# Optimization experiments

Measured on AMD Instinct MI355X. Metric: run time of the kernel, lower is better.

The kernel has to match this reference:

```python
import jax, jax.numpy as jnp
import numpy as np
import math

T = 120      # frame_num == audio_len == max_seq_len
D = 64       # hidden_layer_size
H = 2        # n_head
DH = D // H
DFF = 2 * D
DOUT = 31
PERIOD = 10
EPS = 1e-5
NEG = -1e9
SCALE = 1.0 / math.sqrt(DH)
SLOPES = (1.0 / 16.0, 1.0 / 256.0)  # ALiBi slopes for n_head=2


def _pe():
    # PeriodicPositionalEncoding: sinusoid over one period, tiled
    pos = jnp.arange(PERIOD, dtype=jnp.float32)[:, None]
    div = jnp.exp(jnp.arange(0, D, 2, dtype=jnp.float32) * (-math.log(10000.0) / D))
    s, c = jnp.sin(pos * div), jnp.cos(pos * div)
    pe = jnp.stack([s, c], axis=-1).reshape(PERIOD, D)  # interleave sin/cos
    return jnp.tile(pe, (T // PERIOD + 1, 1))[:T]


def _alibi_mask():
    # causal mask + ALiBi bias: alibi[i,j] = -slope * floor((i-j)/period) for j<=i
    slopes = jnp.array(SLOPES, dtype=jnp.float32)
    i = jnp.arange(T)[:, None]
    j = jnp.arange(T)[None, :]
    rel = ((i - j) // PERIOD).astype(jnp.float32)
    return jnp.where(j <= i, -slopes[:, None, None] * rel, NEG)  # [H,T,T]


def _ln(x, g, b):
    m = x.mean(-1, keepdims=True)
    v = ((x - m) ** 2).mean(-1, keepdims=True)
    return (x - m) / jnp.sqrt(v + EPS) * g + b


def setup_inputs() -> dict:
    key = jax.random.key(0)
    ks = iter(jax.random.split(key, 32))
    n = lambda shape, s=0.05: jax.random.normal(next(ks), shape, dtype=jnp.float32) * s
    inp = {
        'audio': jax.random.normal(next(ks), (1, T, 1024), dtype=jnp.float32),
        'W_audio': n((D, 1024)), 'b_audio': n((D,)),
        'obj_W': n((D, 5)),
        'Wq': n((D, D)), 'bq': n((D,)), 'Wk': n((D, D)), 'bk': n((D,)),
        'Wv': n((D, D)), 'bv': n((D,)), 'Wo': n((D, D)), 'bo': n((D,)),
        'Wv2': n((D, D)), 'bv2': n((D,)), 'Wo2': n((D, D)), 'bo2': n((D,)),
        'g1': jnp.ones((D,)), 'be1': jnp.zeros((D,)),
        'g2': jnp.ones((D,)), 'be2': jnp.zeros((D,)),
        'g3': jnp.ones((D,)), 'be3': jnp.zeros((D,)),
        'W1': n((DFF, D)), 'c1': n((DFF,)), 'W2': n((D, DFF)), 'c2': n((D,)),
        'Wr': n((DOUT, D)), 'br': n((DOUT,)), 'Wm': n((D, DOUT)), 'bm': n((D,)),
    }
    return inp


def _forward(audio, W_audio, b_audio, obj_W, Wq, bq, Wk, bk, Wv, bv, Wo, bo,
             Wv2, bv2, Wo2, bo2, g1, be1, g2, be2, g3, be3,
             W1, c1, W2, c2, Wr, br, Wm, bm):
    mem = audio[0] @ W_audio.T + b_audio          # [S,D], S == T
    style = obj_W[:, 0]                            # obj_vector @ [1,0,0,0,0]
    pe = _pe()
    mask = _alibi_mask()
    slopes = jnp.array(SLOPES, dtype=jnp.float32)
    jarr = jnp.arange(T)

    # enc_dec_mask leaves exactly one memory key per target row (anti-diagonal
    # from the end); the feedback row t at step t always attends memory[-1],
    # so its cross-attn output is just the projected value of the last frame.
    cross_last = (mem[-1] @ Wv2.T + bv2) @ Wo2.T + bo2  # [D]

    def step(emb, t):
        # decode only the last row (row t) of the growing sequence; 1-layer
        # post-norm decoder => row t depends only on input rows 0..t.
        x = emb + pe                                 # PPE over prefix
        xq = jnp.take(x, t, axis=0)                  # [D]
        q = (xq @ Wq.T + bq).reshape(H, DH)
        k = (x @ Wk.T + bk).reshape(T, H, DH)
        v = (x @ Wv.T + bv).reshape(T, H, DH)
        bias = jnp.where(jarr <= t,
                         -slopes[:, None] * ((t - jarr) // PERIOD).astype(jnp.float32),
                         NEG)                        # [H,T]
        sc = jnp.einsum('hd,shd->hs', q, k) * SCALE + bias
        a = jax.nn.softmax(sc, axis=-1)
        sa = jnp.einsum('hs,shd->hd', a, v).reshape(D) @ Wo.T + bo
        h1 = _ln(xq + sa, g1, be1)
        h2 = _ln(h1 + cross_last, g2, be2)
        h3 = _ln(h2 + jax.nn.relu(h2 @ W1.T + c1) @ W2.T + c2, g3, be3)
        new = (h3 @ Wr.T + br) @ Wm.T + bm + style   # vertice_map(vertice_map_r(.)) + style
        emb = jax.lax.dynamic_update_slice(emb, new[None, :], (t + 1, 0))
        return emb, None

    emb0 = jnp.zeros((T, D), audio.dtype).at[0].set(style)
    emb, _ = jax.lax.scan(step, emb0, jnp.arange(T - 1))

    # final full-length decode (last loop iteration of the torch module)
    x = emb + pe
    q = (x @ Wq.T + bq).reshape(T, H, DH)
    k = (x @ Wk.T + bk).reshape(T, H, DH)
    v = (x @ Wv.T + bv).reshape(T, H, DH)
    sc = jnp.einsum('thd,shd->hts', q, k) * SCALE + mask
    a = jax.nn.softmax(sc, axis=-1)
    sa = jnp.einsum('hts,shd->thd', a, v).reshape(T, D) @ Wo.T + bo
    h1 = _ln(x + sa, g1, be1)
    # at length T with S == T the enc_dec_mask aligns target row j <-> memory row j
    cross = (mem @ Wv2.T + bv2) @ Wo2.T + bo2
    h2 = _ln(h1 + cross, g2, be2)
    h3 = _ln(h2 + jax.nn.relu(h2 @ W1.T + c1) @ W2.T + c2, g3, be3)
    return (h3 @ Wr.T + br)[None]                    # [1,T,31]


def reference(audio, W_audio, b_audio, obj_W, Wq, bq, Wk, bk, Wv, bv, Wo, bo,
              Wv2, bv2, Wo2, bo2, g1, be1, g2, be2, g3, be3,
              W1, c1, W2, c2, Wr, br, Wm, bm):
    return _forward(audio, W_audio, b_audio, obj_W, Wq, bq, Wk, bk, Wv, bv, Wo, bo,
                    Wv2, bv2, Wo2, bo2, g1, be1, g2, be2, g3, be3,
                    W1, c1, W2, c2, Wr, br, Wm, bm)
```

## Files before the change

### kernel.cpp

```cpp
#include <hip/hip_runtime.h>

typedef unsigned short u16;
typedef unsigned int   u32;
typedef _Float16 f16;
typedef f16 h2 __attribute__((ext_vector_type(2)));
typedef f16 h4 __attribute__((ext_vector_type(4)));
typedef f16 h8 __attribute__((ext_vector_type(8)));

#define T_    120
#define D_    64
#define DFF_  128
#define DOUT_ 31
#define KROW_ 68
#define VROW_ 132

#if defined(__has_builtin)
#if __has_builtin(__builtin_amdgcn_fdot2)
#define DOT2(a,b,c) __builtin_amdgcn_fdot2((a),(b),(c),false)
#endif
#endif
#ifndef DOT2
#define DOT2(a,b,c) ((float)(a).x*(float)(b).x + ((float)(a).y*(float)(b).y + (c)))
#endif
#define SHV(x,i,j) __builtin_shufflevector((x),(x),(i),(j))

__device__ __forceinline__ h2 pk(float a, float b){
#if defined(__has_builtin) && __has_builtin(__builtin_amdgcn_cvt_pkrtz)
  return __builtin_bit_cast(h2, __builtin_amdgcn_cvt_pkrtz(a, b));
#else
  h2 r; r.x = (f16)a; r.y = (f16)b; return r;
#endif
}

__device__ __forceinline__ float b2f(u16 u){ return __uint_as_float(((u32)u) << 16); }
__device__ __forceinline__ float2 bp2(u32 u){
  float2 r; r.x = __uint_as_float(u << 16); r.y = __uint_as_float(u & 0xffff0000u); return r;
}
__device__ __forceinline__ u16 f2bu(float f){
  u32 u = __float_as_uint(f);
  u32 r = u + 0x7fffu + ((u >> 16) & 1u);
  return (u16)(r >> 16);
}
#define WSYNC() do{ __asm__ __volatile__("" ::: "memory"); __builtin_amdgcn_wave_barrier(); }while(0)

__device__ __forceinline__ float dpp_sum(float x){
  int t;
  t = __builtin_amdgcn_update_dpp(0, __float_as_int(x), 0x111, 0xf, 0xf, true); x += __int_as_float(t);
  t = __builtin_amdgcn_update_dpp(0, __float_as_int(x), 0x112, 0xf, 0xf, true); x += __int_as_float(t);
  t = __builtin_amdgcn_update_dpp(0, __float_as_int(x), 0x114, 0xf, 0xf, true); x += __int_as_float(t);
  t = __builtin_amdgcn_update_dpp(0, __float_as_int(x), 0x118, 0xf, 0xf, true); x += __int_as_float(t);
  t = __builtin_amdgcn_update_dpp(0, __float_as_int(x), 0x142, 0xf, 0xf, true); x += __int_as_float(t);
  t = __builtin_amdgcn_update_dpp(0, __float_as_int(x), 0x143, 0xf, 0xf, true); x += __int_as_float(t);
  return __int_as_float(__builtin_amdgcn_readlane(__float_as_int(x), 63));
}
__device__ __forceinline__ float dpp_max_pos(float x){
  int t;
  t = __builtin_amdgcn_update_dpp(0, __float_as_int(x), 0x111, 0xf, 0xf, true); x = fmaxf(x, __int_as_float(t));
  t = __builtin_amdgcn_update_dpp(0, __float_as_int(x), 0x112, 0xf, 0xf, true); x = fmaxf(x, __int_as_float(t));
  t = __builtin_amdgcn_update_dpp(0, __float_as_int(x), 0x114, 0xf, 0xf, true); x = fmaxf(x, __int_as_float(t));
  t = __builtin_amdgcn_update_dpp(0, __float_as_int(x), 0x118, 0xf, 0xf, true); x = fmaxf(x, __int_as_float(t));
  t = __builtin_amdgcn_update_dpp(0, __float_as_int(x), 0x142, 0xf, 0xf, true); x = fmaxf(x, __int_as_float(t));
  t = __builtin_amdgcn_update_dpp(0, __float_as_int(x), 0x143, 0xf, 0xf, true); x = fmaxf(x, __int_as_float(t));
  return __int_as_float(__builtin_amdgcn_readlane(__float_as_int(x), 63));
}
__device__ __forceinline__ float pe_val(int row, int i){
  const float coef = -0.28782313662425574f;
  int p = row % 10;
  float dv  = __expf((float)(i >> 1) * coef);
  float ang = (float)p * dv;
  return (i & 1) ? __cosf(ang) : __sinf(ang);
}
__device__ __forceinline__ void loadrow32(h2* dst, const float* row){
  #pragma unroll
  for (int r = 0; r < 16; ++r){
    float4 f = ((const float4*)row)[r];
    dst[2*r]   = pk(f.x, f.y);
    dst[2*r+1] = pk(f.z, f.w);
  }
}
__device__ __forceinline__ void loadrow64(h2* dst, const float* row){
  #pragma unroll
  for (int r = 0; r < 32; ++r){
    float4 f = ((const float4*)row)[r];
    dst[2*r]   = pk(f.x, f.y);
    dst[2*r+1] = pk(f.z, f.w);
  }
}

__global__ __launch_bounds__(256) void k_prep(const float* __restrict__ Wv, const float* __restrict__ Wo,
                                              const float* __restrict__ W1, const float* __restrict__ W2,
                                              const float* __restrict__ Wr,
                                              u16* __restrict__ wvb, u16* __restrict__ wob,
                                              u16* __restrict__ w1b, u16* __restrict__ w2b,
                                              u16* __restrict__ wrb){
  int i0 = blockIdx.x*256 + threadIdx.x, stride = gridDim.x*256;
  for (int i = i0; i < 4096; i += stride){ wvb[i] = f2bu(Wv[i]); wob[i] = f2bu(Wo[i]); }
  for (int i = i0; i < 8192; i += stride){ w1b[i] = f2bu(W1[i]); w2b[i] = f2bu(W2[i]); }
  for (int i = i0; i < 1984; i += stride){ wrb[i] = f2bu(Wr[i]); }
}

__global__ __launch_bounds__(256) void k_mem(const float* __restrict__ audio,
                                             const float* __restrict__ Wa,
                                             const float* __restrict__ ba,
                                             float* __restrict__ mem){
  __shared__ float ash[1024];
  const int t = blockIdx.x, tid = threadIdx.x;
  for (int i = tid; i < 1024; i += 256) ash[i] = audio[t*1024 + i];
  __syncthreads();
  const int w = tid >> 6, lane = tid & 63;
  for (int d = w*16; d < w*16 + 16; ++d){
    const float4* row = (const float4*)(Wa + d*1024);
    float acc = 0.f;
    #pragma unroll
    for (int m = 0; m < 4; ++m){
      float4 wp = row[lane + 64*m];
      int j = 4*(lane + 64*m);
      acc += wp.x*ash[j] + wp.y*ash[j+1] + wp.z*ash[j+2] + wp.w*ash[j+3];
    }
    acc = dpp_sum(acc);
    if (lane == 0) mem[t*64 + d] = acc + ba[d];
  }
}

__global__ __launch_bounds__(64) void k_cross(const float* __restrict__ mem,
                                              const float* __restrict__ Wv2, const float* __restrict__ bv2,
                                              const float* __restrict__ Wo2, const float* __restrict__ bo2,
                                              float* __restrict__ cross){
  __shared__ float msh[64], tsh[64];
  const int t = blockIdx.x, i = threadIdx.x;
  msh[i] = mem[t*64 + i];
  __syncthreads();
  const float4* r1 = (const float4*)(Wv2 + i*64);
  float a = bv2[i];
  #pragma unroll
  for (int j = 0; j < 16; ++j){ float4 w = r1[j]; a += w.x*msh[4*j] + w.y*msh[4*j+1] + w.z*msh[4*j+2] + w.w*msh[4*j+3]; }
  tsh[i] = a;
  __syncthreads();
  const float4* r2 = (const float4*)(Wo2 + i*64);
  float c = bo2[i];
  #pragma unroll
  for (int j = 0; j < 16; ++j){ float4 w = r2[j]; c += w.x*tsh[4*j] + w.y*tsh[4*j+1] + w.z*tsh[4*j+2] + w.w*tsh[4*j+3]; }
  cross[t*64 + i] = c;
}

__global__ __launch_bounds__(128, 1) void k_scan(
    const float* __restrict__ objW,
    const float* __restrict__ Wq, const float* __restrict__ bq,
    const float* __restrict__ Wk, const float* __restrict__ bk,
    const float* __restrict__ Wv, const float* __restrict__ bv,
    const float* __restrict__ Wo, const float* __restrict__ bo,
    const float* __restrict__ g1, const float* __restrict__ be1,
    const float* __restrict__ g2, const float* __restrict__ be2,
    const float* __restrict__ g3, const float* __restrict__ be3,
    const float* __restrict__ W1, const float* __restrict__ c1,
    const float* __restrict__ W2, const float* __restrict__ c2,
    const float* __restrict__ Wr, const float* __restrict__ br,
    const float* __restrict__ Wm, const float* __restrict__ bm,
    const float* __restrict__ cross,
    float* __restrict__ xw, float* __restrict__ Kw, float* __restrict__ Vw)
{
  __shared__ __align__(16) f16 KcS[128*KROW_];
  __shared__ __align__(16) f16 VcS[D_*VROW_];
  __shared__ __align__(16) f16 sch[256];
  __shared__ __align__(16) f16 xh[64], qh[64], ath[64], h2h[64], h3h[64], rsh[32];
  __shared__ __align__(16) f16 fsh[128];
  __shared__ float at_p[64];
  __shared__ float pe_tab[640];

  const int tid = threadIdx.x;
  const int i = tid & 63;
  const bool w0 = tid < 64;

  h2 WA[32];
  h2 WB[32];
  h2 WOr[32], W1r[32], WRr[32], WMr[16];
  h2 W2r[64];
  float biasA=0.f, biasB=0.f, bo_r=0.f, c1r=0.f, c2_r=0.f, br_r=0.f, bmst=0.f, cls_r=0.f;
  float g1r=0.f,b1r=0.f,g2r=0.f,b2r=0.f,g3r=0.f,b3r=0.f, xr=0.f;

  if (w0){
    loadrow32(WA,  Wq + i*64);
    loadrow32(WB,  Wv + i*64);
    loadrow32(WOr, Wo + i*64);
    loadrow32(W1r, W1 + i*64);
    loadrow64(W2r, W2 + i*128);
    loadrow32(WRr, Wr + (i < 31 ? i : 30)*64);
    { const float* row = Wm + i*31;
      #pragma unroll
      for (int r = 0; r < 15; ++r) WMr[r] = pk(row[2*r], row[2*r+1]);
      WMr[15] = pk(row[30], 0.f); }
    biasA = bq[i]; biasB = bv[i]; bo_r = bo[i]; c1r = c1[i]; c2_r = c2[i];
    br_r = (i < 31) ? br[i] : 0.f;
    float st = objW[i*5];
    bmst = bm[i] + st;
    cls_r = cross[119*64 + i];
    g1r=g1[i]; b1r=be1[i]; g2r=g2[i]; b2r=be2[i]; g3r=g3[i]; b3r=be3[i];
    xr = st + pe_val(0, i);
    xh[i] = (f16)xr;
    xw[i] = xr;
  } else {
    loadrow32(WA, Wk + i*64);
    loadrow32(WB, W1 + (64+i)*64);
    biasA = bk[i]; c1r = c1[64+i];
  }
  { u32* kcw = (u32*)KcS; for (int idx = tid; idx < 128*KROW_/2; idx += 128) kcw[idx] = 0; }
  { u32* vcw = (u32*)VcS; for (int idx = tid; idx < D_*VROW_/2;  idx += 128) vcw[idx] = 0; }
  for (int idx = tid; idx < 640; idx += 128) pe_tab[idx] = pe_val(idx >> 6, idx & 63);
  if (tid < 32) rsh[tid] = (f16)0.f;
  __syncthreads();

  int pp = 1;
  for (int t = 0; t < T_-1; ++t){
    float atp0 = 0.f;
    {
      const h8* xv = (const h8*)xh;
      float a0=biasA, a1=0.f, a2=0.f, a3=0.f;
      #pragma unroll
      for (int r = 0; r < 8; ++r){
        h8 x = xv[r];
        a0 = DOT2(WA[4*r+0], SHV(x,0,1), a0);
        a1 = DOT2(WA[4*r+1], SHV(x,2,3), a1);
        a2 = DOT2(WA[4*r+2], SHV(x,4,5), a2);
        a3 = DOT2(WA[4*r+3], SHV(x,6,7), a3);
      }
      float accA = (a0+a1)+(a2+a3);
      if (w0){
        float b0=biasB, b1=0.f, b2=0.f, b3=0.f;
        #pragma unroll
        for (int r = 0; r < 8; ++r){
          h8 x = xv[r];
          b0 = DOT2(WB[4*r+0], SHV(x,0,1), b0);
          b1 = DOT2(WB[4*r+1], SHV(x,2,3), b1);
          b2 = DOT2(WB[4*r+2], SHV(x,4,5), b2);
          b3 = DOT2(WB[4*r+3], SHV(x,6,7), b3);
        }
        float accB = (b0+b1)+(b2+b3);
        qh[i] = (f16)accA;
        VcS[i*VROW_ + t] = (f16)accB;
        Vw[t*64 + i] = accB;
      } else {
        KcS[t*KROW_ + i] = (f16)accA;
        Kw[t*64 + i] = accA;
      }
    }
    __syncthreads();
    {
      const int h = tid >> 6, j = i;
      const h8* qv = (const h8*)(qh + h*32);
      const h4* k0 = (const h4*)(KcS + j*KROW_ + h*32);
      const h4* k1 = (const h4*)(KcS + (j+64)*KROW_ + h*32);
      float d0a=0.f,d0b=0.f,d1a=0.f,d1b=0.f;
      #pragma unroll
      for (int r = 0; r < 4; ++r){
        h8 q = qv[r];
        h4 ka = k0[2*r], kb = k0[2*r+1], kc = k1[2*r], kd = k1[2*r+1];
        d0a = DOT2(SHV(ka,0,1), SHV(q,0,1), d0a);
        d0b = DOT2(SHV(ka,2,3), SHV(q,2,3), d0b);
        d0a = DOT2(SHV(kb,0,1), SHV(q,4,5), d0a);
        d0b = DOT2(SHV(kb,2,3), SHV(q,6,7), d0b);
        d1a = DOT2(SHV(kc,0,1), SHV(q,0,1), d1a);
        d1b = DOT2(SHV(kc,2,3), SHV(q,2,3), d1b);
        d1a = DOT2(SHV(kd,0,1), SHV(q,4,5), d1a);
        d1b = DOT2(SHV(kd,2,3), SHV(q,6,7), d1b);
      }
      float d0 = d0a + d0b, d1 = d1a + d1b;
      const float slope = h ? 0.00390625f : 0.0625f;
      int r0 = (t - j) / 10, r1 = (t - j - 64) / 10;
      float s0 = (j      <= t) ? d0*0.17677669529663687f - slope*(float)r0 : -1e30f;
      float s1 = (j + 64 <= t) ? d1*0.17677669529663687f - slope*(float)r1 : -1e30f;
      float m = dpp_max_pos(fmaxf(s0, s1) + 16384.f) - 16384.f;
      float e0 = (j      <= t) ? __expf(s0 - m) : 0.f;
      float e1 = (j + 64 <= t) ? __expf(s1 - m) : 0.f;
      float inv = 1.f / dpp_sum(e0 + e1);
      sch[h*128 + j]      = (f16)(e0*inv);
      sch[h*128 + j + 64] = (f16)(e1*inv);
    }
    __syncthreads();
    {
      const int hd = i >> 5;
      const h8* av = (const h8*)(sch + hd*128) + (w0 ? 0 : 8);
      const h4* vv = (const h4*)(VcS + i*VROW_) + (w0 ? 0 : 16);
      float p0=0.f,p1=0.f,p2=0.f,p3=0.f;
      #pragma unroll
      for (int r = 0; r < 8; ++r){
        h8 a = av[r];
        h4 va = vv[2*r], vb = vv[2*r+1];
        p0 = DOT2(SHV(va,0,1), SHV(a,0,1), p0);
        p1 = DOT2(SHV(va,2,3), SHV(a,2,3), p1);
        p2 = DOT2(SHV(vb,0,1), SHV(a,4,5), p2);
        p3 = DOT2(SHV(vb,2,3), SHV(a,6,7), p3);
      }
      float p = (p0+p1)+(p2+p3);
      if (!w0) at_p[i] = p; else atp0 = p;
    }
    __syncthreads();
    if (w0){
      float atv = atp0 + at_p[i];
      ath[i] = (f16)atv;
      WSYNC();
      const h8* av = (const h8*)ath;
      float a0=bo_r, a1=0.f, a2=0.f, a3=0.f;
      #pragma unroll
      for (int r = 0; r < 8; ++r){
        h8 x = av[r];
        a0 = DOT2(WOr[4*r+0], SHV(x,0,1), a0);
        a1 = DOT2(WOr[4*r+1], SHV(x,2,3), a1);
        a2 = DOT2(WOr[4*r+2], SHV(x,4,5), a2);
        a3 = DOT2(WOr[4*r+3], SHV(x,6,7), a3);
      }
      float y = xr + (a0+a1)+(a2+a3);
      float s = dpp_sum(y), s2 = dpp_sum(y*y);
      float m = s*(1.f/64.f), var = fmaxf(s2*(1.f/64.f) - m*m, 0.f);
      float h1 = (y - m)*rsqrtf(var + 1e-5f)*g1r + b1r;
      float z = h1 + cls_r;
      float sz = dpp_sum(z), sz2 = dpp_sum(z*z);
      float mz = sz*(1.f/64.f), vz = fmaxf(sz2*(1.f/64.f) - mz*mz, 0.f);
      float h2v = (z - mz)*rsqrtf(vz + 1e-5f)*g2r + b2r;
      h2h[i] = (f16)h2v;
      at_p[i] = h2v;
    }
    __syncthreads();
    {
      const h8* hv = (const h8*)h2h;
      float a0=c1r, a1=0.f, a2=0.f, a3=0.f;
      if (w0){
        #pragma unroll
        for (int r = 0; r < 8; ++r){
          h8 x = hv[r];
          a0 = DOT2(W1r[4*r+0], SHV(x,0,1), a0);
          a1 = DOT2(W1r[4*r+1], SHV(x,2,3), a1);
          a2 = DOT2(W1r[4*r+2], SHV(x,4,5), a2);
          a3 = DOT2(W1r[4*r+3], SHV(x,6,7), a3);
        }
      } else {
        #pragma unroll
        for (int r = 0; r < 8; ++r){
          h8 x = hv[r];
          a0 = DOT2(WB[4*r+0], SHV(x,0,1), a0);
          a1 = DOT2(WB[4*r+1], SHV(x,2,3), a1);
          a2 = DOT2(WB[4*r+2], SHV(x,4,5), a2);
          a3 = DOT2(WB[4*r+3], SHV(x,6,7), a3);
        }
      }
      fsh[tid] = (f16)fmaxf((a0+a1)+(a2+a3), 0.f);
    }
    __syncthreads();
    if (w0){
      const h8* fv = (const h8*)fsh;
      float a0=c2_r, a1=0.f, a2=0.f, a3=0.f;
      #pragma unroll
      for (int r = 0; r < 16; ++r){
        h8 x = fv[r];
        a0 = DOT2(W2r[4*r+0], SHV(x,0,1), a0);
        a1 = DOT2(W2r[4*r+1], SHV(x,2,3), a1);
        a2 = DOT2(W2r[4*r+2], SHV(x,4,5), a2);
        a3 = DOT2(W2r[4*r+3], SHV(x,6,7), a3);
      }
      float y = at_p[i] + (a0+a1)+(a2+a3);
      float s = dpp_sum(y), s2 = dpp_sum(y*y);
      float m = s*(1.f/64.f), var = fmaxf(s2*(1.f/64.f) - m*m, 0.f);
      float h3v = (y - m)*rsqrtf(var + 1e-5f)*g3r + b3r;
      h3h[i] = (f16)h3v;
      WSYNC();
      const h8* h3v8 = (const h8*)h3h;
      float r0=br_r, r1=0.f, r2=0.f, r3=0.f;
      #pragma unroll
      for (int r = 0; r < 8; ++r){
        h8 x = h3v8[r];
        r0 = DOT2(WRr[4*r+0], SHV(x,0,1), r0);
        r1 = DOT2(WRr[4*r+1], SHV(x,2,3), r1);
        r2 = DOT2(WRr[4*r+2], SHV(x,4,5), r2);
        r3 = DOT2(WRr[4*r+3], SHV(x,6,7), r3);
      }
      if (i < 31) rsh[i] = (f16)((r0+r1)+(r2+r3));
      WSYNC();
      const h8* rv = (const h8*)rsh;
      float m0=bmst, m1=0.f, m2=0.f, m3=0.f;
      #pragma unroll
      for (int r = 0; r < 4; ++r){
        h8 x = rv[r];
        m0 = DOT2(WMr[4*r+0], SHV(x,0,1), m0);
        m1 = DOT2(WMr[4*r+1], SHV(x,2,3), m1);
        m2 = DOT2(WMr[4*r+2], SHV(x,4,5), m2);
        m3 = DOT2(WMr[4*r+3], SHV(x,6,7), m3);
      }
      float xn = (m0+m1)+(m2+m3) + pe_tab[pp*64 + i];
      xr = xn;
      xh[i] = (f16)xn;
      xw[(t+1)*64 + i] = xn;
    }
    __syncthreads();
    pp = (pp == 9) ? 0 : pp + 1;
  }
  {
    const h8* xv = (const h8*)xh;
    if (w0){
      float b0=biasB, b1=0.f, b2=0.f, b3=0.f;
      #pragma unroll
      for (int r = 0; r < 8; ++r){
        h8 x = xv[r];
        b0 = DOT2(WB[4*r+0], SHV(x,0,1), b0);
        b1 = DOT2(WB[4*r+1], SHV(x,2,3), b1);
        b2 = DOT2(WB[4*r+2], SHV(x,4,5), b2);
        b3 = DOT2(WB[4*r+3], SHV(x,6,7), b3);
      }
      Vw[119*64 + i] = (b0+b1)+(b2+b3);
    } else {
      float a0=biasA, a1=0.f, a2=0.f, a3=0.f;
      #pragma unroll
      for (int r = 0; r < 8; ++r){
        h8 x = xv[r];
        a0 = DOT2(WA[4*r+0], SHV(x,0,1), a0);
        a1 = DOT2(WA[4*r+1], SHV(x,2,3), a1);
        a2 = DOT2(WA[4*r+2], SHV(x,4,5), a2);
        a3 = DOT2(WA[4*r+3], SHV(x,6,7), a3);
      }
      Kw[119*64 + i] = (a0+a1)+(a2+a3);
    }
  }
}

__global__ __launch_bounds__(128) void k_final(
    const float* __restrict__ Wq, const float* __restrict__ bq, const float* __restrict__ bo,
    const float* __restrict__ g1, const float* __restrict__ be1,
    const float* __restrict__ g2, const float* __restrict__ be2,
    const float* __restrict__ g3, const float* __restrict__ be3,
    const float* __restrict__ c1, const float* __restrict__ c2, const float* __restrict__ br,
    const u16* __restrict__ wo_b, const u16* __restrict__ w1_b,
    const u16* __restrict__ w2_b, const u16* __restrict__ wr_b,
    const float* __restrict__ cross, const float* __restrict__ xw,
    const float* __restrict__ Kw, const float* __restrict__ Vw,
    float* __restrict__ out)
{
  __shared__ float xs[64], qs[64], at[64], h2s[64], h3s[64], fs[128], sc[256];
  const int irow = blockIdx.x, tid = threadIdx.x;
  if (tid < 64) xs[tid] = xw[irow*64 + tid];
  __syncthreads();
  if (tid < 64){
    const float4* wr_ = (const float4*)(Wq + tid*64);
    float acc = bq[tid];
    #pragma unroll
    for (int j = 0; j < 16; ++j){ float4 w = wr_[j]; acc += w.x*xs[4*j] + w.y*xs[4*j+1] + w.z*xs[4*j+2] + w.w*xs[4*j+3]; }
    qs[tid] = acc;
  }
  __syncthreads();
  {
    const int h = tid >> 6, j = tid & 63;
    const float* qh_ = qs + h*32;
    float d0 = 0.f, d1 = 0.f;
    const float4* k0 = (const float4*)(Kw + j*64 + h*32);
    #pragma unroll
    for (int w = 0; w < 8; ++w){ float4 p = k0[w]; d0 += p.x*qh_[4*w] + p.y*qh_[4*w+1] + p.z*qh_[4*w+2] + p.w*qh_[4*w+3]; }
    if (j < 56){
      const float4* k1 = (const float4*)(Kw + (j+64)*64 + h*32);
      #pragma unroll
      for (int w = 0; w < 8; ++w){ float4 p = k1[w]; d1 += p.x*qh_[4*w] + p.y*qh_[4*w+1] + p.z*qh_[4*w+2] + p.w*qh_[4*w+3]; }
    }
    const float slope = h ? 0.00390625f : 0.0625f;
    float s0 = (j      <= irow) ? d0*0.17677669529663687f - slope*(float)((irow-j)/10)    : -1e30f;
    float s1 = (j + 64 <= irow) ? d1*0.17677669529663687f - slope*(float)((irow-j-64)/10) : -1e30f;
    float m = dpp_max_pos(fmaxf(s0, s1) + 16384.f) - 16384.f;
    float e0 = (j      <= irow) ? __expf(s0 - m) : 0.f;
    float e1 = (j + 64 <= irow) ? __expf(s1 - m) : 0.f;
    float inv = 1.f / dpp_sum(e0 + e1);
    sc[h*128 + j]      = e0*inv;
    sc[h*128 + j + 64] = e1*inv;
  }
  __syncthreads();
  if (tid < 64){
    const float* a = sc + (tid >> 5)*128;
    float a0=0.f,a1=0.f,a2=0.f,a3=0.f;
    #pragma unroll
    for (int jj = 0; jj < 30; ++jj){
      a0 += a[4*jj]   * Vw[(4*jj)*64   + tid];
      a1 += a[4*jj+1] * Vw[(4*jj+1)*64 + tid];
      a2 += a[4*jj+2] * Vw[(4*jj+2)*64 + tid];
      a3 += a[4*jj+3] * Vw[(4*jj+3)*64 + tid];
    }
    at[tid] = (a0+a1)+(a2+a3);
  }
  __syncthreads();
  if (tid < 64){
    const u32* orow = (const u32*)(wo_b + tid*64);
    float acc = bo[tid];
    #pragma unroll
    for (int w = 0; w < 32; ++w){ float2 p = bp2(orow[w]); acc += p.x*at[2*w] + p.y*at[2*w+1]; }
    float y = xs[tid] + acc;
    float s = dpp_sum(y), s2 = dpp_sum(y*y);
    float m = s*(1.f/64.f), var = fmaxf(s2*(1.f/64.f) - m*m, 0.f);
    float h1 = (y - m)*rsqrtf(var + 1e-5f)*g1[tid] + be1[tid];
    float z = h1 + cross[irow*64 + tid];
    float sz = dpp_sum(z), sz2 = dpp_sum(z*z);
    float mz = sz*(1.f/64.f), vz = fmaxf(sz2*(1.f/64.f) - mz*mz, 0.f);
    h2s[tid] = (z - mz)*rsqrtf(vz + 1e-5f)*g2[tid] + be2[tid];
  }
  __syncthreads();
  {
    const u32* w1r = (const u32*)(w1_b + tid*64);
    float acc = c1[tid];
    #pragma unroll
    for (int w = 0; w < 32; ++w){ float2 p = bp2(w1r[w]); acc += p.x*h2s[2*w] + p.y*h2s[2*w+1]; }
    fs[tid] = fmaxf(acc, 0.f);
  }
  __syncthreads();
  if (tid < 64){
    const u32* w2r = (const u32*)(w2_b + tid*128);
    float acc = c2[tid];
    #pragma unroll
    for (int w = 0; w < 64; ++w){ float2 p = bp2(w2r[w]); acc += p.x*fs[2*w] + p.y*fs[2*w+1]; }
    float y = h2s[tid] + acc;
    float s = dpp_sum(y), s2 = dpp_sum(y*y);
    float m = s*(1.f/64.f), var = fmaxf(s2*(1.f/64.f) - m*m, 0.f);
    h3s[tid] = (y - m)*rsqrtf(var + 1e-5f)*g3[tid] + be3[tid];
  }
  __syncthreads();
  if (tid < DOUT_){
    const u32* rr = (const u32*)(wr_b + tid*64);
    float acc = br[tid];
    #pragma unroll
    for (int w = 0; w < 32; ++w){ float2 p = bp2(rr[w]); acc += p.x*h3s[2*w] + p.y*h3s[2*w+1]; }
    out[irow*DOUT_ + tid] = acc;
  }
}

extern "C" void kernel_launch(void* const* d_in, const int* in_sizes, int n_in,
                              void* d_out, int out_size, void* d_ws, size_t ws_size,
                              hipStream_t stream){
  const float* audio=(const float*)d_in[0];
  const float* Wa   =(const float*)d_in[1];
  const float* ba   =(const float*)d_in[2];
  const float* objW =(const float*)d_in[3];
  const float* Wq   =(const float*)d_in[4];
  const float* bq   =(const float*)d_in[5];
  const float* Wk   =(const float*)d_in[6];
  const float* bk   =(const float*)d_in[7];
  const float* Wv   =(const float*)d_in[8];
  const float* bv   =(const float*)d_in[9];
  const float* Wo   =(const float*)d_in[10];
  const float* bo   =(const float*)d_in[11];
  const float* Wv2  =(const float*)d_in[12];
  const float* bv2  =(const float*)d_in[13];
  const float* Wo2  =(const float*)d_in[14];
  const float* bo2  =(const float*)d_in[15];
  const float* g1   =(const float*)d_in[16];
  const float* be1  =(const float*)d_in[17];
  const float* g2   =(const float*)d_in[18];
  const float* be2  =(const float*)d_in[19];
  const float* g3   =(const float*)d_in[20];
  const float* be3  =(const float*)d_in[21];
  const float* W1   =(const float*)d_in[22];
  const float* c1   =(const float*)d_in[23];
  const float* W2   =(const float*)d_in[24];
  const float* c2   =(const float*)d_in[25];
  const float* Wr   =(const float*)d_in[26];
  const float* br   =(const float*)d_in[27];
  const float* Wm   =(const float*)d_in[28];
  const float* bm   =(const float*)d_in[29];

  float* ws    = (float*)d_ws;
  float* mem   = ws;
  float* cross = ws + 7680;
  float* xw    = ws + 15360;
  float* Kw    = ws + 23040;
  float* Vw    = ws + 30720;
  u16* bb   = (u16*)(ws + 38400);
  u16* wv_b = bb;
  u16* wo_b = bb + 4096;
  u16* w1_b = bb + 8192;
  u16* w2_b = bb + 16384;
  u16* wr_b = bb + 24576;
  float* out = (float*)d_out;

  k_prep <<<dim3(32),  dim3(256), 0, stream>>>(Wv, Wo, W1, W2, Wr, wv_b, wo_b, w1_b, w2_b, wr_b);
  k_mem  <<<dim3(120), dim3(256), 0, stream>>>(audio, Wa, ba, mem);
  k_cross<<<dim3(120), dim3(64),  0, stream>>>(mem, Wv2, bv2, Wo2, bo2, cross);
  k_scan <<<dim3(1),   dim3(128), 0, stream>>>(objW, Wq, bq, Wk, bk, Wv, bv, Wo, bo,
                                               g1, be1, g2, be2, g3, be3,
                                               W1, c1, W2, c2, Wr, br, Wm, bm,
                                               cross, xw, Kw, Vw);
  k_final<<<dim3(120), dim3(128), 0, stream>>>(Wq, bq, bo, g1, be1, g2, be2, g3, be3,
                                               c1, c2, br, wo_b, w1_b, w2_b, wr_b,
                                               cross, xw, Kw, Vw, out);
}
```

Measured before the change: 440.6 us.

## Run serial decode scan on a single wavefront and fuse prep kernels

The sequential scan kernel now runs with one 64-lane wavefront instead of two. Each lane does the Q/K/V, both attention heads, and both FFN halves itself, so every block-wide __syncthreads becomes a wave barrier. Separately, the weight conversion, audio projection and cross-attention kernels are merged into one launch, with an extra block doing the bf16 conversion. The intent is to cut barrier latency on the latency-bound serial loop and drop two kernel launches, at the cost of twice the per-lane arithmetic and much higher register pressure from holding all weight rows per lane.

```diff
diff --git a/kernel.cpp b/kernel.cpp
--- a/kernel.cpp
+++ b/kernel.cpp
@@ -9,7 +9,6 @@
 
 #define T_    120
 #define D_    64
-#define DFF_  128
 #define DOUT_ 31
 #define KROW_ 68
 #define VROW_ 132
@@ -31,7 +30,6 @@
   h2 r; r.x = (f16)a; r.y = (f16)b; return r;
 #endif
 }
-
 __device__ __forceinline__ float b2f(u16 u){ return __uint_as_float(((u32)u) << 16); }
 __device__ __forceinline__ float2 bp2(u32 u){
   float2 r; r.x = __uint_as_float(u << 16); r.y = __uint_as_float(u & 0xffff0000u); return r;
@@ -78,34 +76,26 @@
     dst[2*r+1] = pk(f.z, f.w);
   }
 }
-__device__ __forceinline__ void loadrow64(h2* dst, const float* row){
-  #pragma unroll
-  for (int r = 0; r < 32; ++r){
-    float4 f = ((const float4*)row)[r];
-    dst[2*r]   = pk(f.x, f.y);
-    dst[2*r+1] = pk(f.z, f.w);
-  }
-}
-
-__global__ __launch_bounds__(256) void k_prep(const float* __restrict__ Wv, const float* __restrict__ Wo,
-                                              const float* __restrict__ W1, const float* __restrict__ W2,
-                                              const float* __restrict__ Wr,
-                                              u16* __restrict__ wvb, u16* __restrict__ wob,
-                                              u16* __restrict__ w1b, u16* __restrict__ w2b,
-                                              u16* __restrict__ wrb){
-  int i0 = blockIdx.x*256 + threadIdx.x, stride = gridDim.x*256;
-  for (int i = i0; i < 4096; i += stride){ wvb[i] = f2bu(Wv[i]); wob[i] = f2bu(Wo[i]); }
-  for (int i = i0; i < 8192; i += stride){ w1b[i] = f2bu(W1[i]); w2b[i] = f2bu(W2[i]); }
-  for (int i = i0; i < 1984; i += stride){ wrb[i] = f2bu(Wr[i]); }
-}
-
-__global__ __launch_bounds__(256) void k_mem(const float* __restrict__ audio,
-                                             const float* __restrict__ Wa,
-                                             const float* __restrict__ ba,
-                                             float* __restrict__ mem){
+
+__global__ __launch_bounds__(256) void k_pre(const float* __restrict__ audio,
+                                             const float* __restrict__ Wa, const float* __restrict__ ba,
+                                             const float* __restrict__ Wv2, const float* __restrict__ bv2,
+                                             const float* __restrict__ Wo2, const float* __restrict__ bo2,
+                                             const float* __restrict__ Wo, const float* __restrict__ W1,
+                                             const float* __restrict__ W2, const float* __restrict__ Wr,
+                                             float* __restrict__ cross,
+                                             u16* __restrict__ wob, u16* __restrict__ w1b,
+                                             u16* __restrict__ w2b, u16* __restrict__ wrb){
+  const int b = blockIdx.x, tid = threadIdx.x;
+  if (b == 120){
+    for (int i = tid; i < 4096; i += 256) wob[i] = f2bu(Wo[i]);
+    for (int i = tid; i < 8192; i += 256){ w1b[i] = f2bu(W1[i]); w2b[i] = f2bu(W2[i]); }
+    for (int i = tid; i < 1984; i += 256) wrb[i] = f2bu(Wr[i]);
+    return;
+  }
   __shared__ float ash[1024];
-  const int t = blockIdx.x, tid = threadIdx.x;
-  for (int i = tid; i < 1024; i += 256) ash[i] = audio[t*1024 + i];
+  __shared__ float msh[64], tsh[64];
+  for (int i = tid; i < 1024; i += 256) ash[i] = audio[b*1024 + i];
   __syncthreads();
   const int w = tid >> 6, lane = tid & 63;
   for (int d = w*16; d < w*16 + 16; ++d){
@@ -118,32 +108,27 @@
       acc += wp.x*ash[j] + wp.y*ash[j+1] + wp.z*ash[j+2] + wp.w*ash[j+3];
     }
     acc = dpp_sum(acc);
-    if (lane == 0) mem[t*64 + d] = acc + ba[d];
-  }
-}
-
-__global__ __launch_bounds__(64) void k_cross(const float* __restrict__ mem,
-                                              const float* __restrict__ Wv2, const float* __restrict__ bv2,
-                                              const float* __restrict__ Wo2, const float* __restrict__ bo2,
-                                              float* __restrict__ cross){
-  __shared__ float msh[64], tsh[64];
-  const int t = blockIdx.x, i = threadIdx.x;
-  msh[i] = mem[t*64 + i];
-  __syncthreads();
-  const float4* r1 = (const float4*)(Wv2 + i*64);
-  float a = bv2[i];
-  #pragma unroll
-  for (int j = 0; j < 16; ++j){ float4 w = r1[j]; a += w.x*msh[4*j] + w.y*msh[4*j+1] + w.z*msh[4*j+2] + w.w*msh[4*j+3]; }
-  tsh[i] = a;
-  __syncthreads();
-  const float4* r2 = (const float4*)(Wo2 + i*64);
-  float c = bo2[i];
-  #pragma unroll
-  for (int j = 0; j < 16; ++j){ float4 w = r2[j]; c += w.x*tsh[4*j] + w.y*tsh[4*j+1] + w.z*tsh[4*j+2] + w.w*tsh[4*j+3]; }
-  cross[t*64 + i] = c;
-}
-
-__global__ __launch_bounds__(128, 1) void k_scan(
+    if (lane == 0) msh[d] = acc + ba[d];
+  }
+  __syncthreads();
+  if (tid < 64){
+    const float4* r1 = (const float4*)(Wv2 + tid*64);
+    float a = bv2[tid];
+    #pragma unroll
+    for (int j = 0; j < 16; ++j){ float4 p = r1[j]; a += p.x*msh[4*j] + p.y*msh[4*j+1] + p.z*msh[4*j+2] + p.w*msh[4*j+3]; }
+    tsh[tid] = a;
+  }
+  __syncthreads();
+  if (tid < 64){
+    const float4* r2 = (const float4*)(Wo2 + tid*64);
+    float c = bo2[tid];
+    #pragma unroll
+    for (int j = 0; j < 16; ++j){ float4 p = r2[j]; c += p.x*tsh[4*j] + p.y*tsh[4*j+1] + p.z*tsh[4*j+2] + p.w*tsh[4*j+3]; }
+    cross[b*64 + tid] = c;
+  }
+}
+
+__global__ __launch_bounds__(64, 1) void k_scan(
     const float* __restrict__ objW,
     const float* __restrict__ Wq, const float* __restrict__ bq,
     const float* __restrict__ Wk, const float* __restrict__ bk,
@@ -163,126 +148,132 @@
   __shared__ __align__(16) f16 VcS[D_*VROW_];
   __shared__ __align__(16) f16 sch[256];
   __shared__ __align__(16) f16 xh[64], qh[64], ath[64], h2h[64], h3h[64], rsh[32];
-  __shared__ __align__(16) f16 fsh[128];
-  __shared__ float at_p[64];
+  __shared__ __align__(16) h2  fsh2[64];
   __shared__ float pe_tab[640];
 
-  const int tid = threadIdx.x;
-  const int i = tid & 63;
-  const bool w0 = tid < 64;
-
-  h2 WA[32];
-  h2 WB[32];
-  h2 WOr[32], W1r[32], WRr[32], WMr[16];
+  const int i = threadIdx.x;
+
+  h2 WQ[32], WK[32], WV[32], WOr[32], W1a[32], W1b[32], WRr[32], WMr[16];
   h2 W2r[64];
-  float biasA=0.f, biasB=0.f, bo_r=0.f, c1r=0.f, c2_r=0.f, br_r=0.f, bmst=0.f, cls_r=0.f;
-  float g1r=0.f,b1r=0.f,g2r=0.f,b2r=0.f,g3r=0.f,b3r=0.f, xr=0.f;
-
-  if (w0){
-    loadrow32(WA,  Wq + i*64);
-    loadrow32(WB,  Wv + i*64);
-    loadrow32(WOr, Wo + i*64);
-    loadrow32(W1r, W1 + i*64);
-    loadrow64(W2r, W2 + i*128);
-    loadrow32(WRr, Wr + (i < 31 ? i : 30)*64);
-    { const float* row = Wm + i*31;
-      #pragma unroll
-      for (int r = 0; r < 15; ++r) WMr[r] = pk(row[2*r], row[2*r+1]);
-      WMr[15] = pk(row[30], 0.f); }
-    biasA = bq[i]; biasB = bv[i]; bo_r = bo[i]; c1r = c1[i]; c2_r = c2[i];
-    br_r = (i < 31) ? br[i] : 0.f;
-    float st = objW[i*5];
-    bmst = bm[i] + st;
-    cls_r = cross[119*64 + i];
-    g1r=g1[i]; b1r=be1[i]; g2r=g2[i]; b2r=be2[i]; g3r=g3[i]; b3r=be3[i];
-    xr = st + pe_val(0, i);
-    xh[i] = (f16)xr;
-    xw[i] = xr;
-  } else {
-    loadrow32(WA, Wk + i*64);
-    loadrow32(WB, W1 + (64+i)*64);
-    biasA = bk[i]; c1r = c1[64+i];
-  }
-  { u32* kcw = (u32*)KcS; for (int idx = tid; idx < 128*KROW_/2; idx += 128) kcw[idx] = 0; }
-  { u32* vcw = (u32*)VcS; for (int idx = tid; idx < D_*VROW_/2;  idx += 128) vcw[idx] = 0; }
-  for (int idx = tid; idx < 640; idx += 128) pe_tab[idx] = pe_val(idx >> 6, idx & 63);
-  if (tid < 32) rsh[tid] = (f16)0.f;
-  __syncthreads();
+
+  loadrow32(WQ,  Wq + i*64);
+  loadrow32(WK,  Wk + i*64);
+  loadrow32(WV,  Wv + i*64);
+  loadrow32(WOr, Wo + i*64);
+  loadrow32(W1a, W1 + i*64);
+  loadrow32(W1b, W1 + (64+i)*64);
+  {
+    const float4* ra = (const float4*)(W2 + i*128);
+    const float4* rb = (const float4*)(W2 + i*128 + 64);
+    #pragma unroll
+    for (int r = 0; r < 16; ++r){
+      float4 a = ra[r], b = rb[r];
+      W2r[4*r+0] = pk(a.x, b.x); W2r[4*r+1] = pk(a.y, b.y);
+      W2r[4*r+2] = pk(a.z, b.z); W2r[4*r+3] = pk(a.w, b.w);
+    }
+  }
+  loadrow32(WRr, Wr + (i < 31 ? i : 30)*64);
+  {
+    const float* row = Wm + i*31;
+    #pragma unroll
+    for (int r = 0; r < 15; ++r) WMr[r] = pk(row[2*r], row[2*r+1]);
+    WMr[15] = pk(row[30], 0.f);
+  }
+  const float bq_r = bq[i], bk_r = bk[i], bv_r = bv[i], bo_r = bo[i];
+  const float c1a = c1[i], c1b = c1[64+i], c2_r = c2[i];
+  const float br_r = (i < 31) ? br[i] : 0.f;
+  const float st = objW[i*5];
+  const float bmst = bm[i] + st;
+  const float cls_r = cross[119*64 + i];
+  const float g1r = g1[i], b1r = be1[i], g2r = g2[i], b2r = be2[i], g3r = g3[i], b3r = be3[i];
+
+  { u32* p = (u32*)KcS; for (int idx = i; idx < 128*KROW_/2; idx += 64) p[idx] = 0; }
+  { u32* p = (u32*)VcS; for (int idx = i; idx < D_*VROW_/2;  idx += 64) p[idx] = 0; }
+  for (int idx = i; idx < 640; idx += 64) pe_tab[idx] = pe_val(idx >> 6, idx & 63);
+  if (i < 32) rsh[i] = (f16)0.f;
+
+  float xr = st + pe_val(0, i);
+  xh[i] = (f16)xr;
+  xw[i] = xr;
+  WSYNC();
 
   int pp = 1;
   for (int t = 0; t < T_-1; ++t){
-    float atp0 = 0.f;
     {
       const h8* xv = (const h8*)xh;
-      float a0=biasA, a1=0.f, a2=0.f, a3=0.f;
+      float q0=bq_r,q1=0.f,q2=0.f,q3=0.f, k0=bk_r,k1=0.f,k2=0.f,k3=0.f, v0=bv_r,v1=0.f,v2=0.f,v3=0.f;
       #pragma unroll
       for (int r = 0; r < 8; ++r){
         h8 x = xv[r];
-        a0 = DOT2(WA[4*r+0], SHV(x,0,1), a0);
-        a1 = DOT2(WA[4*r+1], SHV(x,2,3), a1);
-        a2 = DOT2(WA[4*r+2], SHV(x,4,5), a2);
-        a3 = DOT2(WA[4*r+3], SHV(x,6,7), a3);
-      }
-      float accA = (a0+a1)+(a2+a3);
-      if (w0){
-        float b0=biasB, b1=0.f, b2=0.f, b3=0.f;
-        #pragma unroll
-        for (int r = 0; r < 8; ++r){
-          h8 x = xv[r];
-          b0 = DOT2(WB[4*r+0], SHV(x,0,1), b0);
-          b1 = DOT2(WB[4*r+1], SHV(x,2,3), b1);
-          b2 = DOT2(WB[4*r+2], SHV(x,4,5), b2);
-          b3 = DOT2(WB[4*r+3], SHV(x,6,7), b3);
-        }
-        float accB = (b0+b1)+(b2+b3);
-        qh[i] = (f16)accA;
-        VcS[i*VROW_ + t] = (f16)accB;
-        Vw[t*64 + i] = accB;
-      } else {
-        KcS[t*KROW_ + i] = (f16)accA;
-        Kw[t*64 + i] = accA;
-      }
-    }
-    __syncthreads();
-    {
-      const int h = tid >> 6, j = i;
-      const h8* qv = (const h8*)(qh + h*32);
-      const h4* k0 = (const h4*)(KcS + j*KROW_ + h*32);
-      const h4* k1 = (const h4*)(KcS + (j+64)*KROW_ + h*32);
-      float d0a=0.f,d0b=0.f,d1a=0.f,d1b=0.f;
+        h2 xa=SHV(x,0,1), xb=SHV(x,2,3), xc=SHV(x,4,5), xd=SHV(x,6,7);
+        q0 = DOT2(WQ[4*r+0], xa, q0); q1 = DOT2(WQ[4*r+1], xb, q1);
+        q2 = DOT2(WQ[4*r+2], xc, q2); q3 = DOT2(WQ[4*r+3], xd, q3);
+        k0 = DOT2(WK[4*r+0], xa, k0); k1 = DOT2(WK[4*r+1], xb, k1);
+        k2 = DOT2(WK[4*r+2], xc, k2); k3 = DOT2(WK[4*r+3], xd, k3);
+        v0 = DOT2(WV[4*r+0], xa, v0); v1 = DOT2(WV[4*r+1], xb, v1);
+        v2 = DOT2(WV[4*r+2], xc, v2); v3 = DOT2(WV[4*r+3], xd, v3);
+      }
+      float q = (q0+q1)+(q2+q3), k = (k0+k1)+(k2+k3), v = (v0+v1)+(v2+v3);
+      qh[i] = (f16)q;
+      KcS[t*KROW_ + i] = (f16)k;
+      VcS[i*VROW_ + t] = (f16)v;
+      Kw[t*64 + i] = k;
+      Vw[t*64 + i] = v;
+    }
+    WSYNC();
+    {
+      const int j = i;
+      const h8* qv = (const h8*)qh;
+      const h4* kr0 = (const h4*)(KcS + j*KROW_);
+      const h4* kr1 = (const h4*)(KcS + (j+64)*KROW_);
+      float a00=0.f,b00=0.f,a01=0.f,b01=0.f,a10=0.f,b10=0.f,a11=0.f,b11=0.f;
       #pragma unroll
       for (int r = 0; r < 4; ++r){
-        h8 q = qv[r];
-        h4 ka = k0[2*r], kb = k0[2*r+1], kc = k1[2*r], kd = k1[2*r+1];
-        d0a = DOT2(SHV(ka,0,1), SHV(q,0,1), d0a);
-        d0b = DOT2(SHV(ka,2,3), SHV(q,2,3), d0b);
-        d0a = DOT2(SHV(kb,0,1), SHV(q,4,5), d0a);
-        d0b = DOT2(SHV(kb,2,3), SHV(q,6,7), d0b);
-        d1a = DOT2(SHV(kc,0,1), SHV(q,0,1), d1a);
-        d1b = DOT2(SHV(kc,2,3), SHV(q,2,3), d1b);
-        d1a = DOT2(SHV(kd,0,1), SHV(q,4,5), d1a);
-        d1b = DOT2(SHV(kd,2,3), SHV(q,6,7), d1b);
-      }
-      float d0 = d0a + d0b, d1 = d1a + d1b;
-      const float slope = h ? 0.00390625f : 0.0625f;
+        h8 qlo = qv[r], qhi = qv[4+r];
+        h2 ql0=SHV(qlo,0,1), ql1=SHV(qlo,2,3), ql2=SHV(qlo,4,5), ql3=SHV(qlo,6,7);
+        h2 qh0=SHV(qhi,0,1), qh1=SHV(qhi,2,3), qh2=SHV(qhi,4,5), qh3=SHV(qhi,6,7);
+        h4 ka = kr0[2*r], kb = kr0[2*r+1];
+        h4 kc = kr0[8+2*r], kd = kr0[9+2*r];
+        h4 ke = kr1[2*r], kf = kr1[2*r+1];
+        h4 kg = kr1[8+2*r], kh = kr1[9+2*r];
+        a00 = DOT2(SHV(ka,0,1), ql0, a00); b00 = DOT2(SHV(ka,2,3), ql1, b00);
+        a00 = DOT2(SHV(kb,0,1), ql2, a00); b00 = DOT2(SHV(kb,2,3), ql3, b00);
+        a10 = DOT2(SHV(kc,0,1), qh0, a10); b10 = DOT2(SHV(kc,2,3), qh1, b10);
+        a10 = DOT2(SHV(kd,0,1), qh2, a10); b10 = DOT2(SHV(kd,2,3), qh3, b10);
+        a01 = DOT2(SHV(ke,0,1), ql0, a01); b01 = DOT2(SHV(ke,2,3), ql1, b01);
+        a01 = DOT2(SHV(kf,0,1), ql2, a01); b01 = DOT2(SHV(kf,2,3), ql3, b01);
+        a11 = DOT2(SHV(kg,0,1), qh0, a11); b11 = DOT2(SHV(kg,2,3), qh1, b11);
+        a11 = DOT2(SHV(kh,0,1), qh2, a11); b11 = DOT2(SHV(kh,2,3), qh3, b11);
+      }
+      float d00 = a00+b00, d01 = a01+b01, d10 = a10+b10, d11 = a11+b11;
+      const float SC = 0.17677669529663687f;
       int r0 = (t - j) / 10, r1 = (t - j - 64) / 10;
-      float s0 = (j      <= t) ? d0*0.17677669529663687f - slope*(float)r0 : -1e30f;
-      float s1 = (j + 64 <= t) ? d1*0.17677669529663687f - slope*(float)r1 : -1e30f;
-      float m = dpp_max_pos(fmaxf(s0, s1) + 16384.f) - 16384.f;
-      float e0 = (j      <= t) ? __expf(s0 - m) : 0.f;
-      float e1 = (j + 64 <= t) ? __expf(s1 - m) : 0.f;
-      float inv = 1.f / dpp_sum(e0 + e1);
-      sch[h*128 + j]      = (f16)(e0*inv);
-      sch[h*128 + j + 64] = (f16)(e1*inv);
-    }
-    __syncthreads();
-    {
-      const int hd = i >> 5;
-      const h8* av = (const h8*)(sch + hd*128) + (w0 ? 0 : 8);
-      const h4* vv = (const h4*)(VcS + i*VROW_) + (w0 ? 0 : 16);
+      bool m0v = (j <= t), m1v = (j + 64 <= t);
+      float s00 = m0v ? d00*SC - 0.0625f*(float)r0      : -1e30f;
+      float s01 = m1v ? d01*SC - 0.0625f*(float)r1      : -1e30f;
+      float s10 = m0v ? d10*SC - 0.00390625f*(float)r0  : -1e30f;
+      float s11 = m1v ? d11*SC - 0.00390625f*(float)r1  : -1e30f;
+      float mx0 = dpp_max_pos(fmaxf(s00, s01) + 16384.f) - 16384.f;
+      float mx1 = dpp_max_pos(fmaxf(s10, s11) + 16384.f) - 16384.f;
+      float e00 = m0v ? __expf(s00 - mx0) : 0.f;
+      float e01 = m1v ? __expf(s01 - mx0) : 0.f;
+      float e10 = m0v ? __expf(s10 - mx1) : 0.f;
+      float e11 = m1v ? __expf(s11 - mx1) : 0.f;
+      float inv0 = 1.f / dpp_sum(e00 + e01);
+      float inv1 = 1.f / dpp_sum(e10 + e11);
+      sch[j]        = (f16)(e00*inv0);
+      sch[j+64]     = (f16)(e01*inv0);
+      sch[128+j]    = (f16)(e10*inv1);
+      sch[128+j+64] = (f16)(e11*inv1);
+    }
+    WSYNC();
+    float atv;
+    {
+      const h8* av = (const h8*)(sch + (i >> 5)*128);
+      const h4* vv = (const h4*)(VcS + i*VROW_);
       float p0=0.f,p1=0.f,p2=0.f,p3=0.f;
       #pragma unroll
-      for (int r = 0; r < 8; ++r){
+      for (int r = 0; r < 15; ++r){
         h8 a = av[r];
         h4 va = vv[2*r], vb = vv[2*r+1];
         p0 = DOT2(SHV(va,0,1), SHV(a,0,1), p0);
@@ -290,14 +281,12 @@
         p2 = DOT2(SHV(vb,0,1), SHV(a,4,5), p2);
         p3 = DOT2(SHV(vb,2,3), SHV(a,6,7), p3);
       }
-      float p = (p0+p1)+(p2+p3);
-      if (!w0) at_p[i] = p; else atp0 = p;
-    }
-    __syncthreads();
-    if (w0){
-      float atv = atp0 + at_p[i];
+      atv = (p0+p1)+(p2+p3);
       ath[i] = (f16)atv;
-      WSYNC();
+    }
+    WSYNC();
+    float h2v;
+    {
       const h8* av = (const h8*)ath;
       float a0=bo_r, a1=0.f, a2=0.f, a3=0.f;
       #pragma unroll
@@ -315,38 +304,30 @@
       float z = h1 + cls_r;
       float sz = dpp_sum(z), sz2 = dpp_sum(z*z);
       float mz = sz*(1.f/64.f), vz = fmaxf(sz2*(1.f/64.f) - mz*mz, 0.f);
-      float h2v = (z - mz)*rsqrtf(vz + 1e-5f)*g2r + b2r;
+      h2v = (z - mz)*rsqrtf(vz + 1e-5f)*g2r + b2r;
       h2h[i] = (f16)h2v;
-      at_p[i] = h2v;
-    }
-    __syncthreads();
+    }
+    WSYNC();
     {
       const h8* hv = (const h8*)h2h;
-      float a0=c1r, a1=0.f, a2=0.f, a3=0.f;
-      if (w0){
-        #pragma unroll
-        for (int r = 0; r < 8; ++r){
-          h8 x = hv[r];
-          a0 = DOT2(W1r[4*r+0], SHV(x,0,1), a0);
-          a1 = DOT2(W1r[4*r+1], SHV(x,2,3), a1);
-          a2 = DOT2(W1r[4*r+2], SHV(x,4,5), a2);
-          a3 = DOT2(W1r[4*r+3], SHV(x,6,7), a3);
-        }
-      } else {
-        #pragma unroll
-        for (int r = 0; r < 8; ++r){
-          h8 x = hv[r];
-          a0 = DOT2(WB[4*r+0], SHV(x,0,1), a0);
-          a1 = DOT2(WB[4*r+1], SHV(x,2,3), a1);
-          a2 = DOT2(WB[4*r+2], SHV(x,4,5), a2);
-          a3 = DOT2(WB[4*r+3], SHV(x,6,7), a3);
-        }
-      }
-      fsh[tid] = (f16)fmaxf((a0+a1)+(a2+a3), 0.f);
-    }
-    __syncthreads();
-    if (w0){
-      const h8* fv = (const h8*)fsh;
+      float a0=c1a, a1=0.f, a2=0.f, a3=0.f, b0=c1b, b1=0.f, b2=0.f, b3=0.f;
+      #pragma unroll
+      for (int r = 0; r < 8; ++r){
+        h8 x = hv[r];
+        h2 xa=SHV(x,0,1), xb=SHV(x,2,3), xc=SHV(x,4,5), xd=SHV(x,6,7);
+        a0 = DOT2(W1a[4*r+0], xa, a0); a1 = DOT2(W1a[4*r+1], xb, a1);
+        a2 = DOT2(W1a[4*r+2], xc, a2); a3 = DOT2(W1a[4*r+3], xd, a3);
+        b0 = DOT2(W1b[4*r+0], xa, b0); b1 = DOT2(W1b[4*r+1], xb, b1);
+        b2 = DOT2(W1b[4*r+2], xc, b2); b3 = DOT2(W1b[4*r+3], xd, b3);
+      }
+      float fa = fmaxf((a0+a1)+(a2+a3), 0.f);
+      float fb = fmaxf((b0+b1)+(b2+b3), 0.f);
+      fsh2[i] = pk(fa, fb);
+    }
+    WSYNC();
+    float h3v;
+    {
+      const h8* fv = (const h8*)fsh2;
       float a0=c2_r, a1=0.f, a2=0.f, a3=0.f;
       #pragma unroll
       for (int r = 0; r < 16; ++r){
@@ -356,24 +337,28 @@
         a2 = DOT2(W2r[4*r+2], SHV(x,4,5), a2);
         a3 = DOT2(W2r[4*r+3], SHV(x,6,7), a3);
       }
-      float y = at_p[i] + (a0+a1)+(a2+a3);
+      float y = h2v + (a0+a1)+(a2+a3);
       float s = dpp_sum(y), s2 = dpp_sum(y*y);
       float m = s*(1.f/64.f), var = fmaxf(s2*(1.f/64.f) - m*m, 0.f);
-      float h3v = (y - m)*rsqrtf(var + 1e-5f)*g3r + b3r;
+      h3v = (y - m)*rsqrtf(var + 1e-5f)*g3r + b3r;
       h3h[i] = (f16)h3v;
-      WSYNC();
-      const h8* h3v8 = (const h8*)h3h;
+    }
+    WSYNC();
+    {
+      const h8* hv = (const h8*)h3h;
       float r0=br_r, r1=0.f, r2=0.f, r3=0.f;
       #pragma unroll
       for (int r = 0; r < 8; ++r){
-        h8 x = h3v8[r];
+        h8 x = hv[r];
         r0 = DOT2(WRr[4*r+0], SHV(x,0,1), r0);
         r1 = DOT2(WRr[4*r+1], SHV(x,2,3), r1);
         r2 = DOT2(WRr[4*r+2], SHV(x,4,5), r2);
         r3 = DOT2(WRr[4*r+3], SHV(x,6,7), r3);
       }
-      if (i < 31) rsh[i] = (f16)((r0+r1)+(r2+r3));
-      WSYNC();
+      if (i < DOUT_) rsh[i] = (f16)((r0+r1)+(r2+r3));
+    }
+    WSYNC();
+    {
       const h8* rv = (const h8*)rsh;
       float m0=bmst, m1=0.f, m2=0.f, m3=0.f;
       #pragma unroll
@@ -389,34 +374,23 @@
       xh[i] = (f16)xn;
       xw[(t+1)*64 + i] = xn;
     }
-    __syncthreads();
+    WSYNC();
     pp = (pp == 9) ? 0 : pp + 1;
   }
   {
     const h8* xv = (const h8*)xh;
-    if (w0){
-      float b0=biasB, b1=0.f, b2=0.f, b3=0.f;
-      #pragma unroll
-      for (int r = 0; r < 8; ++r){
-        h8 x = xv[r];
-        b0 = DOT2(WB[4*r+0], SHV(x,0,1), b0);
-        b1 = DOT2(WB[4*r+1], SHV(x,2,3), b1);
-        b2 = DOT2(WB[4*r+2], SHV(x,4,5), b2);
-        b3 = DOT2(WB[4*r+3], SHV(x,6,7), b3);
-      }
-      Vw[119*64 + i] = (b0+b1)+(b2+b3);
-    } else {
-      float a0=biasA, a1=0.f, a2=0.f, a3=0.f;
-      #pragma unroll
-      for (int r = 0; r < 8; ++r){
-        h8 x = xv[r];
-        a0 = DOT2(WA[4*r+0], SHV(x,0,1), a0);
-        a1 = DOT2(WA[4*r+1], SHV(x,2,3), a1);
-        a2 = DOT2(WA[4*r+2], SHV(x,4,5), a2);
-        a3 = DOT2(WA[4*r+3], SHV(x,6,7), a3);
-      }
-      Kw[119*64 + i] = (a0+a1)+(a2+a3);
-    }
+    float k0=bk_r,k1=0.f,k2=0.f,k3=0.f, v0=bv_r,v1=0.f,v2=0.f,v3=0.f;
+    #pragma unroll
+    for (int r = 0; r < 8; ++r){
+      h8 x = xv[r];
+      h2 xa=SHV(x,0,1), xb=SHV(x,2,3), xc=SHV(x,4,5), xd=SHV(x,6,7);
+      k0 = DOT2(WK[4*r+0], xa, k0); k1 = DOT2(WK[4*r+1], xb, k1);
+      k2 = DOT2(WK[4*r+2], xc, k2); k3 = DOT2(WK[4*r+3], xd, k3);
+      v0 = DOT2(WV[4*r+0], xa, v0); v1 = DOT2(WV[4*r+1], xb, v1);
+      v2 = DOT2(WV[4*r+2], xc, v2); v3 = DOT2(WV[4*r+3], xd, v3);
+    }
+    Kw[119*64 + i] = (k0+k1)+(k2+k3);
+    Vw[119*64 + i] = (v0+v1)+(v2+v3);
   }
 }
 
@@ -558,23 +532,21 @@
   const float* bm   =(const float*)d_in[29];
 
   float* ws    = (float*)d_ws;
-  float* mem   = ws;
-  float* cross = ws + 7680;
-  float* xw    = ws + 15360;
-  float* Kw    = ws + 23040;
-  float* Vw    = ws + 30720;
-  u16* bb   = (u16*)(ws + 38400);
-  u16* wv_b = bb;
-  u16* wo_b = bb + 4096;
-  u16* w1_b = bb + 8192;
-  u16* w2_b = bb + 16384;
-  u16* wr_b = bb + 24576;
+  float* cross = ws;
+  float* xw    = ws + 7680;
+  float* Kw    = ws + 15360;
+  float* Vw    = ws + 23040;
+  u16* bb   = (u16*)(ws + 30720);
+  u16* wo_b = bb;
+  u16* w1_b = bb + 4096;
+  u16* w2_b = bb + 12288;
+  u16* wr_b = bb + 20480;
   float* out = (float*)d_out;
 
-  k_prep <<<dim3(32),  dim3(256), 0, stream>>>(Wv, Wo, W1, W2, Wr, wv_b, wo_b, w1_b, w2_b, wr_b);
-  k_mem  <<<dim3(120), dim3(256), 0, stream>>>(audio, Wa, ba, mem);
-  k_cross<<<dim3(120), dim3(64),  0, stream>>>(mem, Wv2, bv2, Wo2, bo2, cross);
-  k_scan <<<dim3(1),   dim3(128), 0, stream>>>(objW, Wq, bq, Wk, bk, Wv, bv, Wo, bo,
+  k_pre  <<<dim3(121), dim3(256), 0, stream>>>(audio, Wa, ba, Wv2, bv2, Wo2, bo2,
+                                               Wo, W1, W2, Wr,
+                                               cross, wo_b, w1_b, w2_b, wr_b);
+  k_scan <<<dim3(1),   dim3(64),  0, stream>>>(objW, Wq, bq, Wk, bk, Wv, bv, Wo, bo,
                                                g1, be1, g2, be2, g3, be3,
                                                W1, c1, W2, c2, Wr, br, Wm, bm,
                                                cross, xw, Kw, Vw);
```

After: 632.9 us. +43.7%, slower.
